# Kernel optimization log

Measured on AMD Instinct MI355X. Metric: run time of the kernel, lower is better.

## Reference

```python
import jax, jax.numpy as jnp
import numpy as np
from jax import lax

B, T, D_IN, H, L, D_OUT = 64, 512, 256, 1024, 3, 128


def setup_inputs() -> dict:
    key = jax.random.key(0)
    ks = jax.random.split(key, 8)
    s_in = 1.0 / np.sqrt(H)  # PyTorch-style uniform-ish scale, keeps ReLU recurrence stable
    return {
        "x": jax.random.normal(ks[0], (B, T, D_IN), jnp.float32),
        "w_ih0": jax.random.normal(ks[1], (H, D_IN), jnp.float32) * s_in,
        "w_ih_rest": jax.random.normal(ks[2], (L - 1, H, H), jnp.float32) * s_in,
        "w_hh": jax.random.normal(ks[3], (L, H, H), jnp.float32) * s_in,
        "b_ih": jax.random.normal(ks[4], (L, H), jnp.float32) * s_in,
        "b_hh": jax.random.normal(ks[5], (L, H), jnp.float32) * s_in,
        "fc_w": jax.random.normal(ks[6], (D_OUT, H), jnp.float32) * s_in,
        "fc_b": jax.random.normal(ks[7], (D_OUT,), jnp.float32) * s_in,
    }


def _rnn_layer(seq, w_ih, w_hh, bi, bh):
    # seq: [B, T, d_in]; precompute input projection as one big GEMM
    pre = jnp.einsum("btd,hd->bth", seq, w_ih) + bi + bh  # [B, T, H]
    h0 = jnp.zeros((seq.shape[0], w_hh.shape[0]), seq.dtype)

    def step(h, p_t):  # h: [B, H], p_t: [B, H]
        h = jax.nn.relu(p_t + h @ w_hh.T)
        return h, h

    _, hs = lax.scan(step, h0, jnp.swapaxes(pre, 0, 1))  # [T, B, H]
    return jnp.swapaxes(hs, 0, 1)  # [B, T, H]


def reference(x, w_ih0, w_ih_rest, w_hh, b_ih, b_hh, fc_w, fc_b):
    seq = _rnn_layer(x, w_ih0, w_hh[0], b_ih[0], b_hh[0])
    for l in range(1, L):
        seq = _rnn_layer(seq, w_ih_rest[l - 1], w_hh[l], b_ih[l], b_hh[l])
    # fc on last timestep: out[:, -1, :] @ fc_w.T + fc_b
    return seq[:, -1, :] @ fc_w.T + fc_b
```

## Files before the change

### kernel.cpp

```cpp
#include <hip/hip_runtime.h>

#define NB   64
#define NT   512
#define DIN  256
#define NH   1024
#define DOUT 128

#define HS2_STR 1156
#define RD_STR  136

typedef float f4 __attribute__((ext_vector_type(4)));
typedef unsigned short bfr;

__device__ __forceinline__ float b2f(bfr u) {
    union { unsigned u; float f; } v; v.u = ((unsigned)u) << 16; return v.f;
}
__device__ __forceinline__ bfr f2b(float f) {
    union { float f; unsigned u; } v; v.f = f;
    unsigned r = v.u + 0x7FFFu + ((v.u >> 16) & 1u);
    return (bfr)(r >> 16);
}

template <typename T> __device__ __forceinline__ f4 load4(const T* p);
template <> __device__ __forceinline__ f4 load4<float>(const float* p) { return *(const f4*)p; }
template <> __device__ __forceinline__ f4 load4<bfr>(const bfr* p) {
    ushort4 u = *(const ushort4*)p;
    f4 r; r[0] = b2f(u.x); r[1] = b2f(u.y); r[2] = b2f(u.z); r[3] = b2f(u.w); return r;
}
template <typename T> __device__ __forceinline__ void store1(T* p, float v);
template <> __device__ __forceinline__ void store1<float>(float* p, float v) { *p = v; }
template <> __device__ __forceinline__ void store1<bfr>(bfr* p, float v) { *p = f2b(v); }
template <typename T> __device__ __forceinline__ float load1(const T* p);
template <> __device__ __forceinline__ float load1<float>(const float* p) { return *p; }
template <> __device__ __forceinline__ float load1<bfr>(const bfr* p) { return b2f(*p); }

template <int K, int LOG2CT, typename TA, typename TO>
__global__ __launch_bounds__(256)
void proj_kernel(const TA* __restrict__ A, const float* __restrict__ W,
                 const float* __restrict__ bih, const float* __restrict__ bhh,
                 TO* __restrict__ out, int tOff)
{
    __shared__ float As[16][68];
    __shared__ float Ws[16][68];
    const int tid = threadIdx.x;
    const int CTM = (1 << LOG2CT) - 1;
    const int m0 = (blockIdx.x >> 4) << 6;
    const int n0 = (blockIdx.x & 15) << 6;
    const int tm = tid & 15, tn = tid >> 4;
    const int lr = tid >> 2, lc = tid & 3;

    const int rA = m0 + lr;
    const long mrowA = (long)(rA >> LOG2CT) * NT + tOff + (rA & CTM);

    float acc[4][4] = {};
    for (int k0 = 0; k0 < K; k0 += 16) {
        f4 av = load4<TA>(&A[mrowA * K + k0 + lc * 4]);
        f4 wv = *(const f4*)&W[(n0 + lr) * K + k0 + lc * 4];
        __syncthreads();
        #pragma unroll
        for (int j = 0; j < 4; ++j) {
            As[lc * 4 + j][lr] = av[j];
            Ws[lc * 4 + j][lr] = wv[j];
        }
        __syncthreads();
        #pragma unroll
        for (int k = 0; k < 16; ++k) {
            f4 a = *(const f4*)&As[k][tm * 4];
            f4 w = *(const f4*)&Ws[k][tn * 4];
            #pragma unroll
            for (int i = 0; i < 4; ++i)
                #pragma unroll
                for (int j = 0; j < 4; ++j)
                    acc[i][j] += a[i] * w[j];
        }
    }
    #pragma unroll
    for (int j = 0; j < 4; ++j) {
        const int n = n0 + tn * 4 + j;
        const float bias = bih[n] + bhh[n];
        #pragma unroll
        for (int i = 0; i < 4; ++i)
            store1<TO>(&out[(long)(m0 + tm * 4 + i) * NH + n], acc[i][j] + bias);
    }
}

template <typename TP, int L2CT>
__global__ __launch_bounds__(256)
void copyback_kernel(const TP* __restrict__ Q, TP* __restrict__ P, int tOff)
{
    const int r = blockIdx.x, tid = threadIdx.x;
    const int b = r >> L2CT, t = r & ((1 << L2CT) - 1);
    const TP* q = Q + (long)r * NH;
    TP* p = P + ((long)b * NT + tOff + t) * NH;
    #pragma unroll
    for (int j = 0; j < 4; ++j) p[tid + j * 256] = q[tid + j * 256];
}

__device__ __forceinline__ void poll64(const unsigned* fl, unsigned tgt, int lane)
{
    const unsigned long long* fp = (const unsigned long long*)fl + lane;
    for (;;) {
        unsigned long long v = __hip_atomic_load(fp, __ATOMIC_RELAXED,
                                                 __HIP_MEMORY_SCOPE_AGENT);
        unsigned lo = (unsigned)v, hi = (unsigned)(v >> 32);
        if (__all((int)(lo >= tgt && hi >= tgt))) break;
        __builtin_amdgcn_s_sleep(1);
    }
}

template <typename TP>
__global__ __launch_bounds__(512)
void recur_kernel(const float* __restrict__ Whh, TP* __restrict__ P,
                  float* __restrict__ Hring, unsigned* __restrict__ sy)
{
    __shared__ float hsA[8 * HS2_STR];
    __shared__ float hsB[8 * HS2_STR];
    __shared__ float red[32 * RD_STR];

    const int tid  = threadIdx.x;
    const int wg   = blockIdx.x;
    const int nBase = (wg & 63) << 4;
    const int set   = wg >> 6;
    const int rank  = wg & 63;
    const int lane  = tid & 63;
    const int tk = tid >> 4, tn = (tid >> 1) & 7, tb = tid & 1;
    const int bl = tid >> 4, nl = tid & 15;
    const int srow = tid >> 6;
    const int sgOff = srow * NH + lane * 4;
    const int slOff = srow * HS2_STR + lane * 4 + ((lane >> 3) << 2);

    unsigned* syA = sy + (set * 2 + 0) * 128;
    unsigned* syB = sy + (set * 2 + 1) * 128;
    float* HrA = Hring + (long)(set * 16) * NH;
    float* HrB = HrA + 8 * NH;

    float w0[32], w1[32];
    {
        const float* p0 = &Whh[(nBase + tn * 2 + 0) * NH + tk * 32];
        const float* p1 = &Whh[(nBase + tn * 2 + 1) * NH + tk * 32];
        #pragma unroll
        for (int i = 0; i < 8; ++i) {
            *(f4*)&w0[i * 4] = *(const f4*)&p0[i * 4];
            *(f4*)&w1[i * 4] = *(const f4*)&p1[i * 4];
        }
    }
    for (int i = tid; i < 8 * HS2_STR; i += 512) { hsA[i] = 0.f; hsB[i] = 0.f; }
    __syncthreads();

    #pragma unroll 1
    for (int ts = 0; ts < NT; ++ts) {
        const int slot = (ts & 1) * (NB * NH);
        const int pslot = ((ts - 1) & 1) * (NB * NH);

        float preA = 0.f, preB = 0.f; TP *ppA = nullptr, *ppB = nullptr;
        if (tid < 128) {
            ppA = &P[((long)(set * 16 + bl) * NT + ts) * NH + nBase + nl];
            ppB = &P[((long)(set * 16 + 8 + bl) * NT + ts) * NH + nBase + nl];
            preA = load1<TP>(ppA);
            preB = load1<TP>(ppB);
        }

        float accA[4][2] = {};
        #pragma unroll
        for (int kk = 0; kk < 8; ++kk) {
            const int kko = tk * 36 + kk * 4;
            f4 hv[4];
            #pragma unroll
            for (int i = 0; i < 4; ++i)
                hv[i] = *(const f4*)&hsA[(tb * 4 + i) * HS2_STR + kko];
            #pragma unroll
            for (int c = 0; c < 4; ++c)
                #pragma unroll
                for (int i = 0; i < 4; ++i) {
                    accA[i][0] += hv[i][c] * w0[kk * 4 + c];
                    accA[i][1] += hv[i][c] * w1[kk * 4 + c];
                }
        }

        f4 sB[4];
        if (ts > 0) {
            poll64(syB, (unsigned)ts, lane);
            const float* src = HrB + pslot + sgOff;
            #pragma unroll
            for (int q = 0; q < 4; ++q)
                asm volatile("global_load_dwordx4 %0, %1, off sc0 sc1"
                             : "=v"(sB[q]) : "v"(src + q * 256) : "memory");
        }

        #pragma unroll
        for (int i = 0; i < 4; ++i) {
            float* rp = &red[tk * RD_STR + (tb * 4 + i) * 16 + tn * 2];
            rp[0] = accA[i][0]; rp[1] = accA[i][1];
        }
        __syncthreads();

        if (tid < 128) {
            float s = 0.f;
            #pragma unroll
            for (int q = 0; q < 32; ++q) s += red[q * RD_STR + tid];
            const float h = fmaxf(s + preA, 0.f);
            store1<TP>(ppA, h);
            __hip_atomic_store(&HrA[slot + bl * NH + nBase + nl], h,
                               __ATOMIC_RELAXED, __HIP_MEMORY_SCOPE_AGENT);
            if (ts < NT - 1) {
                asm volatile("s_waitcnt vmcnt(0)" ::: "memory");
                if (lane == 0)
                    __hip_atomic_store(&syA[rank * 2 + (tid >> 6)], (unsigned)(ts + 1),
                                       __ATOMIC_RELAXED, __HIP_MEMORY_SCOPE_AGENT);
            }
        }

        if (ts > 0) {
            asm volatile("s_waitcnt vmcnt(0)" ::: "memory");
            #pragma unroll
            for (int q = 0; q < 4; ++q)
                *(f4*)&hsB[slOff + q * 288] = sB[q];
        }
        __syncthreads();

        float accB[4][2] = {};
        #pragma unroll
        for (int kk = 0; kk < 8; ++kk) {
            const int kko = tk * 36 + kk * 4;
            f4 hv[4];
            #pragma unroll
            for (int i = 0; i < 4; ++i)
                hv[i] = *(const f4*)&hsB[(tb * 4 + i) * HS2_STR + kko];
            #pragma unroll
            for (int c = 0; c < 4; ++c)
                #pragma unroll
                for (int i = 0; i < 4; ++i) {
                    accB[i][0] += hv[i][c] * w0[kk * 4 + c];
                    accB[i][1] += hv[i][c] * w1[kk * 4 + c];
                }
        }

        f4 sA[4];
        if (ts < NT - 1) {
            poll64(syA, (unsigned)(ts + 1), lane);
            const float* src = HrA + slot + sgOff;
            #pragma unroll
            for (int q = 0; q < 4; ++q)
                asm volatile("global_load_dwordx4 %0, %1, off sc0 sc1"
                             : "=v"(sA[q]) : "v"(src + q * 256) : "memory");
        }

        #pragma unroll
        for (int i = 0; i < 4; ++i) {
            float* rp = &red[tk * RD_STR + (tb * 4 + i) * 16 + tn * 2];
            rp[0] = accB[i][0]; rp[1] = accB[i][1];
        }
        __syncthreads();

        if (tid < 128) {
            float s = 0.f;
            #pragma unroll
            for (int q = 0; q < 32; ++q) s += red[q * RD_STR + tid];
            const float h = fmaxf(s + preB, 0.f);
            store1<TP>(ppB, h);
            __hip_atomic_store(&HrB[slot + bl * NH + nBase + nl], h,
                               __ATOMIC_RELAXED, __HIP_MEMORY_SCOPE_AGENT);
            if (ts < NT - 1) {
                asm volatile("s_waitcnt vmcnt(0)" ::: "memory");
                if (lane == 0)
                    __hip_atomic_store(&syB[rank * 2 + (tid >> 6)], (unsigned)(ts + 1),
                                       __ATOMIC_RELAXED, __HIP_MEMORY_SCOPE_AGENT);
            }
        }
        if (ts == NT - 1) break;

        asm volatile("s_waitcnt vmcnt(0)" ::: "memory");
        #pragma unroll
        for (int q = 0; q < 4; ++q)
            *(f4*)&hsA[slOff + q * 288] = sA[q];
        __syncthreads();
    }
}

template <typename TP>
__global__ __launch_bounds__(128)
void fc_kernel(const TP* __restrict__ seq, const float* __restrict__ fcw,
               const float* __restrict__ fcb, float* __restrict__ out)
{
    __shared__ float hrow[NH];
    const int b = blockIdx.x, tid = threadIdx.x;
    for (int i = tid * 4; i < NH; i += 128 * 4) {
        f4 v = load4<TP>(&seq[((long)b * NT + (NT - 1)) * NH + i]);
        *(f4*)&hrow[i] = v;
    }
    __syncthreads();
    float s = 0.f;
    const float* wr = &fcw[tid * NH];
    for (int k = 0; k < NH; k += 4) {
        f4 w = *(const f4*)&wr[k];
        s += w[0] * hrow[k] + w[1] * hrow[k + 1] + w[2] * hrow[k + 2] + w[3] * hrow[k + 3];
    }
    out[b * DOUT + tid] = s + fcb[tid];
}

template <typename TP>
static void coop_recur(const float* W, TP* P, float* Hring, unsigned* sy,
                       hipStream_t stream)
{
    hipMemsetAsync(sy, 0, 4096, stream);
    const float* Wp = W; TP* Pp = P; float* H = Hring; unsigned* s = sy;
    void* args[4] = { &Wp, &Pp, &H, &s };
    hipLaunchCooperativeKernel((const void*)recur_kernel<TP>, dim3(256), dim3(512),
                               args, 0, stream);
}

static void run_pathA(const float* x, const float* wih0, const float* wihr,
                      const float* whh, const float* bih, const float* bhh,
                      const float* fcw, const float* fcb, float* out,
                      unsigned* sy, float* Hring, float* P0, float* P1,
                      hipStream_t stream)
{
    const dim3 blk(256);
    proj_kernel<DIN, 9, float, float><<<8192, blk, 0, stream>>>(x, wih0, bih, bhh, P0, 0);
    coop_recur<float>(whh, P0, Hring, sy, stream);
    proj_kernel<NH, 9, float, float><<<8192, blk, 0, stream>>>(P0, wihr,
        bih + NH, bhh + NH, P1, 0);
    coop_recur<float>(whh + NH * NH, P1, Hring, sy, stream);
    proj_kernel<NH, 9, float, float><<<8192, blk, 0, stream>>>(P1, wihr + NH * NH,
        bih + 2 * NH, bhh + 2 * NH, P0, 0);
    coop_recur<float>(whh + 2 * (NH * NH), P0, Hring, sy, stream);
    fc_kernel<float><<<dim3(NB), dim3(128), 0, stream>>>(P0, fcw, fcb, out);
}

template <typename TP>
static void run_pathBC(const float* x, const float* wih0, const float* wihr,
                       const float* whh, const float* bih, const float* bhh,
                       const float* fcw, const float* fcb, float* out,
                       unsigned* sy, float* Hring, TP* P, TP* Q, hipStream_t stream)
{
    const dim3 blk(256);
    proj_kernel<DIN, 9, float, TP><<<8192, blk, 0, stream>>>(x, wih0, bih, bhh, P, 0);
    coop_recur<TP>(whh, P, Hring, sy, stream);
    for (int l = 1; l < 3; ++l) {
        const float* wih = wihr + (long)(l - 1) * NH * NH;
        for (int c = 0; c < NT / 32; ++c) {
            proj_kernel<NH, 5, TP, TP><<<512, blk, 0, stream>>>(P, wih, bih + l * NH,
                                                                bhh + l * NH, Q, c * 32);
            copyback_kernel<TP, 5><<<NB * 32, blk, 0, stream>>>(Q, P, c * 32);
        }
        coop_recur<TP>(whh + (long)l * NH * NH, P, Hring, sy, stream);
    }
    fc_kernel<TP><<<dim3(NB), dim3(128), 0, stream>>>(P, fcw, fcb, out);
}

extern "C" void kernel_launch(void* const* d_in, const int* in_sizes, int n_in,
                              void* d_out, int out_size, void* d_ws, size_t ws_size,
                              hipStream_t stream)
{
    (void)in_sizes; (void)n_in; (void)out_size;
    const float* x    = (const float*)d_in[0];
    const float* wih0 = (const float*)d_in[1];
    const float* wihr = (const float*)d_in[2];
    const float* whh  = (const float*)d_in[3];
    const float* bih  = (const float*)d_in[4];
    const float* bhh  = (const float*)d_in[5];
    const float* fcw  = (const float*)d_in[6];
    const float* fcb  = (const float*)d_in[7];
    float* out = (float*)d_out;

    char* ws = (char*)d_ws;
    unsigned* sy = (unsigned*)ws;
    float* Hring = (float*)(ws + 4096);
    char* base = ws + 4096 + 2ull * NB * NH * 4;

    const size_t pF32 = (size_t)NB * NT * NH * 4;
    const size_t qF32 = (size_t)NB * 32 * NH * 4;
    const size_t head = 4096 + 2ull * NB * NH * 4;
    const size_t needA = head + 2 * pF32;
    const size_t needB = head + pF32 + qF32;

    if (ws_size >= needA) {
        float* P0 = (float*)base;
        float* P1 = (float*)(base + pF32);
        run_pathA(x, wih0, wihr, whh, bih, bhh, fcw, fcb, out,
                  sy, Hring, P0, P1, stream);
    } else if (ws_size >= needB) {
        float* P = (float*)base;
        float* Q = (float*)(base + pF32);
        run_pathBC<float>(x, wih0, wihr, whh, bih, bhh, fcw, fcb, out,
                          sy, Hring, P, Q, stream);
    } else {
        bfr* P = (bfr*)base;
        bfr* Q = (bfr*)(base + pF32 / 2);
        run_pathBC<bfr>(x, wih0, wihr, whh, bih, bhh, fcw, fcb, out,
                        sy, Hring, P, Q, stream);
    }
}
```

Baseline: 10.90 ms.

## Fuse all three RNN layers into one wavefront-pipelined cooperative kernel with fp16 state

Replaces the per-layer projection GEMMs and three separate cooperative recurrence launches with one cooperative kernel. It runs the three layers as a diagonal wavefront, with layer l at step g-l, and computes the layer 1 and 2 input projections inline using register-resident W_ih slices. Hidden states are exchanged between workgroups as packed fp16 instead of fp32, which halves the ring traffic and LDS footprint. This removes the large intermediate projection GEMMs, the P buffer round trips and two kernel launches. The cost is three times the per-thread weight registers (160 floats), extra flag polling per step, and reduced precision in the recurrent state.

```diff
diff --git a/kernel.cpp b/kernel.cpp
--- a/kernel.cpp
+++ b/kernel.cpp
@@ -5,9 +5,7 @@
 #define DIN  256
 #define NH   1024
 #define DOUT 128
-
-#define HS2_STR 1156
-#define RD_STR  136
+#define NSTEP (NT + 2)
 
 typedef float f4 __attribute__((ext_vector_type(4)));
 typedef unsigned short bfr;
@@ -19,6 +17,14 @@
     union { float f; unsigned u; } v; v.f = f;
     unsigned r = v.u + 0x7FFFu + ((v.u >> 16) & 1u);
     return (bfr)(r >> 16);
+}
+__device__ __forceinline__ unsigned packh(float a, float b) {
+    union { ushort s; _Float16 f; } x, y;
+    x.f = (_Float16)a; y.f = (_Float16)b;
+    return (unsigned)x.s | ((unsigned)y.s << 16);
+}
+__device__ __forceinline__ float h2f(ushort u) {
+    union { ushort s; _Float16 f; } x; x.s = u; return (float)x.f;
 }
 
 template <typename T> __device__ __forceinline__ f4 load4(const T* p);
@@ -34,27 +40,23 @@
 template <> __device__ __forceinline__ float load1<float>(const float* p) { return *p; }
 template <> __device__ __forceinline__ float load1<bfr>(const bfr* p) { return b2f(*p); }
 
-template <int K, int LOG2CT, typename TA, typename TO>
+template <int K, typename TA, typename TO>
 __global__ __launch_bounds__(256)
 void proj_kernel(const TA* __restrict__ A, const float* __restrict__ W,
                  const float* __restrict__ bih, const float* __restrict__ bhh,
-                 TO* __restrict__ out, int tOff)
+                 TO* __restrict__ out)
 {
     __shared__ float As[16][68];
     __shared__ float Ws[16][68];
     const int tid = threadIdx.x;
-    const int CTM = (1 << LOG2CT) - 1;
     const int m0 = (blockIdx.x >> 4) << 6;
     const int n0 = (blockIdx.x & 15) << 6;
     const int tm = tid & 15, tn = tid >> 4;
     const int lr = tid >> 2, lc = tid & 3;
 
-    const int rA = m0 + lr;
-    const long mrowA = (long)(rA >> LOG2CT) * NT + tOff + (rA & CTM);
-
     float acc[4][4] = {};
     for (int k0 = 0; k0 < K; k0 += 16) {
-        f4 av = load4<TA>(&A[mrowA * K + k0 + lc * 4]);
+        f4 av = load4<TA>(&A[(long)(m0 + lr) * K + k0 + lc * 4]);
         f4 wv = *(const f4*)&W[(n0 + lr) * K + k0 + lc * 4];
         __syncthreads();
         #pragma unroll
@@ -84,18 +86,6 @@
     }
 }
 
-template <typename TP, int L2CT>
-__global__ __launch_bounds__(256)
-void copyback_kernel(const TP* __restrict__ Q, TP* __restrict__ P, int tOff)
-{
-    const int r = blockIdx.x, tid = threadIdx.x;
-    const int b = r >> L2CT, t = r & ((1 << L2CT) - 1);
-    const TP* q = Q + (long)r * NH;
-    TP* p = P + ((long)b * NT + tOff + t) * NH;
-    #pragma unroll
-    for (int j = 0; j < 4; ++j) p[tid + j * 256] = q[tid + j * 256];
-}
-
 __device__ __forceinline__ void poll64(const unsigned* fl, unsigned tgt, int lane)
 {
     const unsigned long long* fp = (const unsigned long long*)fl + lane;
@@ -108,185 +98,227 @@
     }
 }
 
-template <typename TP>
+__device__ __forceinline__ float mixrow(const ushort* hbase, const float* w, float acc)
+{
+    const uint4* hp = (const uint4*)hbase;
+    uint4 c0 = hp[0], c1 = hp[1], c2 = hp[2], c3 = hp[3];
+    unsigned uu[16] = { c0.x, c0.y, c0.z, c0.w, c1.x, c1.y, c1.z, c1.w,
+                        c2.x, c2.y, c2.z, c2.w, c3.x, c3.y, c3.z, c3.w };
+    #pragma unroll
+    for (int j = 0; j < 16; ++j) {
+        union { unsigned u; _Float16 h[2]; } t; t.u = uu[j];
+        acc = fmaf((float)t.h[0], w[2 * j + 0], acc);
+        acc = fmaf((float)t.h[1], w[2 * j + 1], acc);
+    }
+    return acc;
+}
+
+template <typename TP0>
 __global__ __launch_bounds__(512)
-void recur_kernel(const float* __restrict__ Whh, TP* __restrict__ P,
-                  float* __restrict__ Hring, unsigned* __restrict__ sy)
-{
-    __shared__ float hsA[8 * HS2_STR];
-    __shared__ float hsB[8 * HS2_STR];
-    __shared__ float red[32 * RD_STR];
+void fused_kernel(const float* __restrict__ whh, const float* __restrict__ wih1,
+                  const float* __restrict__ wih2, const float* __restrict__ bih,
+                  const float* __restrict__ bhh, const TP0* __restrict__ P0,
+                  ushort* __restrict__ Hr, unsigned* __restrict__ sy)
+{
+    __shared__ ushort hs0[16 * NH];
+    __shared__ ushort hs1[16 * NH];
+    __shared__ ushort hs2[16 * NH];
+    __shared__ float red[32][260];
 
     const int tid  = threadIdx.x;
     const int wg   = blockIdx.x;
-    const int nBase = (wg & 63) << 4;
-    const int set   = wg >> 6;
-    const int rank  = wg & 63;
-    const int lane  = tid & 63;
-    const int tk = tid >> 4, tn = (tid >> 1) & 7, tb = tid & 1;
-    const int bl = tid >> 4, nl = tid & 15;
-    const int srow = tid >> 6;
-    const int sgOff = srow * NH + lane * 4;
-    const int slOff = srow * HS2_STR + lane * 4 + ((lane >> 3) << 2);
-
-    unsigned* syA = sy + (set * 2 + 0) * 128;
-    unsigned* syB = sy + (set * 2 + 1) * 128;
-    float* HrA = Hring + (long)(set * 16) * NH;
-    float* HrB = HrA + 8 * NH;
-
-    float w0[32], w1[32];
+    const int rank = wg & 63, set = wg >> 6, lane = tid & 63;
+    const int nBase = rank << 4;
+    const int tk = tid >> 4, tn = tid & 15;
+    const int ko = tk << 5;
+
+    float w0[32], wA[32], w1[32], wB[32], w2[32];
     {
-        const float* p0 = &Whh[(nBase + tn * 2 + 0) * NH + tk * 32];
-        const float* p1 = &Whh[(nBase + tn * 2 + 1) * NH + tk * 32];
+        const long ro = (long)(nBase + tn) * NH + ko;
         #pragma unroll
-        for (int i = 0; i < 8; ++i) {
-            *(f4*)&w0[i * 4] = *(const f4*)&p0[i * 4];
-            *(f4*)&w1[i * 4] = *(const f4*)&p1[i * 4];
-        }
-    }
-    for (int i = tid; i < 8 * HS2_STR; i += 512) { hsA[i] = 0.f; hsB[i] = 0.f; }
+        for (int j = 0; j < 8; ++j) {
+            *(f4*)&w0[j * 4] = *(const f4*)&whh[ro + j * 4];
+            *(f4*)&w1[j * 4] = *(const f4*)&whh[(long)NH * NH + ro + j * 4];
+            *(f4*)&w2[j * 4] = *(const f4*)&whh[2L * NH * NH + ro + j * 4];
+            *(f4*)&wA[j * 4] = *(const f4*)&wih1[ro + j * 4];
+            *(f4*)&wB[j * 4] = *(const f4*)&wih2[ro + j * 4];
+        }
+    }
+    const int rb = tid >> 3, rp = tid & 7;
+    const int n2 = nBase + rp * 2;
+    float bs10 = 0, bs11 = 0, bs20 = 0, bs21 = 0;
+    if (tid < 128) {
+        bs10 = bih[NH + n2] + bhh[NH + n2];
+        bs11 = bih[NH + n2 + 1] + bhh[NH + n2 + 1];
+        bs20 = bih[2 * NH + n2] + bhh[2 * NH + n2];
+        bs21 = bih[2 * NH + n2 + 1] + bhh[2 * NH + n2 + 1];
+    }
+    for (int i = tid; i < 16 * NH / 2; i += 512) {
+        ((unsigned*)hs0)[i] = 0; ((unsigned*)hs1)[i] = 0; ((unsigned*)hs2)[i] = 0;
+    }
     __syncthreads();
 
+    unsigned* fl0 = sy + (set * 3 + 0) * 128;
+    unsigned* fl1 = sy + (set * 3 + 1) * 128;
+    unsigned* fl2 = sy + (set * 3 + 2) * 128;
+    ushort* H0 = Hr;
+    ushort* H1 = Hr + 2 * 65536;
+    ushort* H2 = Hr + 4 * 65536;
+    const int sOff = set * 16384 + tid * 32;
+    const long pBase = ((long)set * 16 + rb) * NT;
+    const int oIdx = rb * 16 + rp * 2;
+
     #pragma unroll 1
-    for (int ts = 0; ts < NT; ++ts) {
-        const int slot = (ts & 1) * (NB * NH);
-        const int pslot = ((ts - 1) & 1) * (NB * NH);
-
-        float preA = 0.f, preB = 0.f; TP *ppA = nullptr, *ppB = nullptr;
-        if (tid < 128) {
-            ppA = &P[((long)(set * 16 + bl) * NT + ts) * NH + nBase + nl];
-            ppB = &P[((long)(set * 16 + 8 + bl) * NT + ts) * NH + nBase + nl];
-            preA = load1<TP>(ppA);
-            preB = load1<TP>(ppB);
-        }
-
-        float accA[4][2] = {};
-        #pragma unroll
-        for (int kk = 0; kk < 8; ++kk) {
-            const int kko = tk * 36 + kk * 4;
-            f4 hv[4];
-            #pragma unroll
-            for (int i = 0; i < 4; ++i)
-                hv[i] = *(const f4*)&hsA[(tb * 4 + i) * HS2_STR + kko];
-            #pragma unroll
-            for (int c = 0; c < 4; ++c)
-                #pragma unroll
-                for (int i = 0; i < 4; ++i) {
-                    accA[i][0] += hv[i][c] * w0[kk * 4 + c];
-                    accA[i][1] += hv[i][c] * w1[kk * 4 + c];
-                }
-        }
-
-        f4 sB[4];
-        if (ts > 0) {
-            poll64(syB, (unsigned)ts, lane);
-            const float* src = HrB + pslot + sgOff;
+    for (int g = 0; g < NSTEP; ++g) {
+        const int slot = g & 1, oslot = slot ^ 1;
+        const bool a0 = (g <= NT - 1);
+        const bool a1 = (g >= 1) && (g <= NT);
+        const bool a2 = (g >= 2) && (g <= NT + 1);
+        const bool sg1 = (g >= 2) && (g <= NT + 1);
+        const bool sg2 = (g >= 3) && (g <= NT + 1);
+        const bool sg0 = (g <= NT - 1);
+        float acc[16];
+        f4 st[4];
+
+        float p00 = 0.f, p01 = 0.f;
+        if (a0 && tid < 128) {
+            const long pa = (pBase + g) * NH + n2;
+            p00 = load1<TP0>(&P0[pa]); p01 = load1<TP0>(&P0[pa + 1]);
+        }
+        if (a0) {
+            #pragma unroll
+            for (int b = 0; b < 16; ++b)
+                acc[b] = mixrow(&hs0[b * NH + ko], w0, 0.f);
+        }
+        if (sg1) {
+            poll64(fl1, (unsigned)g, lane);
+            const char* sp = (const char*)(H1 + oslot * 65536 + sOff);
             #pragma unroll
             for (int q = 0; q < 4; ++q)
                 asm volatile("global_load_dwordx4 %0, %1, off sc0 sc1"
-                             : "=v"(sB[q]) : "v"(src + q * 256) : "memory");
-        }
-
-        #pragma unroll
-        for (int i = 0; i < 4; ++i) {
-            float* rp = &red[tk * RD_STR + (tb * 4 + i) * 16 + tn * 2];
-            rp[0] = accA[i][0]; rp[1] = accA[i][1];
-        }
-        __syncthreads();
-
-        if (tid < 128) {
-            float s = 0.f;
-            #pragma unroll
-            for (int q = 0; q < 32; ++q) s += red[q * RD_STR + tid];
-            const float h = fmaxf(s + preA, 0.f);
-            store1<TP>(ppA, h);
-            __hip_atomic_store(&HrA[slot + bl * NH + nBase + nl], h,
-                               __ATOMIC_RELAXED, __HIP_MEMORY_SCOPE_AGENT);
-            if (ts < NT - 1) {
-                asm volatile("s_waitcnt vmcnt(0)" ::: "memory");
-                if (lane == 0)
-                    __hip_atomic_store(&syA[rank * 2 + (tid >> 6)], (unsigned)(ts + 1),
-                                       __ATOMIC_RELAXED, __HIP_MEMORY_SCOPE_AGENT);
+                             : "=v"(st[q]) : "v"(sp + q * 16) : "memory");
+        }
+        if (a0) {
+            #pragma unroll
+            for (int b = 0; b < 16; ++b) red[tk][b * 16 + tn] = acc[b];
+        }
+        __syncthreads();
+        if (a0 && tid < 128) {
+            float s0 = 0.f, s1 = 0.f;
+            #pragma unroll
+            for (int q = 0; q < 32; ++q) { s0 += red[q][oIdx]; s1 += red[q][oIdx + 1]; }
+            const float v0 = fmaxf(s0 + p00, 0.f), v1 = fmaxf(s1 + p01, 0.f);
+            __hip_atomic_store((unsigned*)(H0 + slot * 65536 + ((set * 16 + rb) << 10) + n2),
+                               packh(v0, v1), __ATOMIC_RELAXED, __HIP_MEMORY_SCOPE_AGENT);
+            asm volatile("s_waitcnt vmcnt(0)" ::: "memory");
+            if (lane == 0)
+                __hip_atomic_store(&fl0[rank * 2 + (tid >> 6)], (unsigned)(g + 1),
+                                   __ATOMIC_RELAXED, __HIP_MEMORY_SCOPE_AGENT);
+        }
+        if (sg1) {
+            asm volatile("s_waitcnt vmcnt(0)" ::: "memory");
+            char* dp = (char*)hs1 + tid * 64;
+            #pragma unroll
+            for (int q = 0; q < 4; ++q) *(f4*)(dp + q * 16) = st[q];
+        }
+        __syncthreads();
+
+        if (a1) {
+            #pragma unroll
+            for (int b = 0; b < 16; ++b) {
+                float a = mixrow(&hs0[b * NH + ko], wA, 0.f);
+                acc[b] = mixrow(&hs1[b * NH + ko], w1, a);
             }
         }
-
-        if (ts > 0) {
-            asm volatile("s_waitcnt vmcnt(0)" ::: "memory");
-            #pragma unroll
-            for (int q = 0; q < 4; ++q)
-                *(f4*)&hsB[slOff + q * 288] = sB[q];
-        }
-        __syncthreads();
-
-        float accB[4][2] = {};
-        #pragma unroll
-        for (int kk = 0; kk < 8; ++kk) {
-            const int kko = tk * 36 + kk * 4;
-            f4 hv[4];
-            #pragma unroll
-            for (int i = 0; i < 4; ++i)
-                hv[i] = *(const f4*)&hsB[(tb * 4 + i) * HS2_STR + kko];
-            #pragma unroll
-            for (int c = 0; c < 4; ++c)
-                #pragma unroll
-                for (int i = 0; i < 4; ++i) {
-                    accB[i][0] += hv[i][c] * w0[kk * 4 + c];
-                    accB[i][1] += hv[i][c] * w1[kk * 4 + c];
-                }
-        }
-
-        f4 sA[4];
-        if (ts < NT - 1) {
-            poll64(syA, (unsigned)(ts + 1), lane);
-            const float* src = HrA + slot + sgOff;
+        if (sg2) {
+            poll64(fl2, (unsigned)g, lane);
+            const char* sp = (const char*)(H2 + oslot * 65536 + sOff);
             #pragma unroll
             for (int q = 0; q < 4; ++q)
                 asm volatile("global_load_dwordx4 %0, %1, off sc0 sc1"
-                             : "=v"(sA[q]) : "v"(src + q * 256) : "memory");
-        }
-
-        #pragma unroll
-        for (int i = 0; i < 4; ++i) {
-            float* rp = &red[tk * RD_STR + (tb * 4 + i) * 16 + tn * 2];
-            rp[0] = accB[i][0]; rp[1] = accB[i][1];
-        }
-        __syncthreads();
-
-        if (tid < 128) {
-            float s = 0.f;
-            #pragma unroll
-            for (int q = 0; q < 32; ++q) s += red[q * RD_STR + tid];
-            const float h = fmaxf(s + preB, 0.f);
-            store1<TP>(ppB, h);
-            __hip_atomic_store(&HrB[slot + bl * NH + nBase + nl], h,
-                               __ATOMIC_RELAXED, __HIP_MEMORY_SCOPE_AGENT);
-            if (ts < NT - 1) {
-                asm volatile("s_waitcnt vmcnt(0)" ::: "memory");
-                if (lane == 0)
-                    __hip_atomic_store(&syB[rank * 2 + (tid >> 6)], (unsigned)(ts + 1),
-                                       __ATOMIC_RELAXED, __HIP_MEMORY_SCOPE_AGENT);
+                             : "=v"(st[q]) : "v"(sp + q * 16) : "memory");
+        }
+        if (a1) {
+            #pragma unroll
+            for (int b = 0; b < 16; ++b) red[tk][b * 16 + tn] = acc[b];
+        }
+        __syncthreads();
+        if (a1 && tid < 128) {
+            float s0 = 0.f, s1 = 0.f;
+            #pragma unroll
+            for (int q = 0; q < 32; ++q) { s0 += red[q][oIdx]; s1 += red[q][oIdx + 1]; }
+            const float v0 = fmaxf(s0 + bs10, 0.f), v1 = fmaxf(s1 + bs11, 0.f);
+            __hip_atomic_store((unsigned*)(H1 + slot * 65536 + ((set * 16 + rb) << 10) + n2),
+                               packh(v0, v1), __ATOMIC_RELAXED, __HIP_MEMORY_SCOPE_AGENT);
+            asm volatile("s_waitcnt vmcnt(0)" ::: "memory");
+            if (lane == 0)
+                __hip_atomic_store(&fl1[rank * 2 + (tid >> 6)], (unsigned)(g + 1),
+                                   __ATOMIC_RELAXED, __HIP_MEMORY_SCOPE_AGENT);
+        }
+        if (sg2) {
+            asm volatile("s_waitcnt vmcnt(0)" ::: "memory");
+            char* dp = (char*)hs2 + tid * 64;
+            #pragma unroll
+            for (int q = 0; q < 4; ++q) *(f4*)(dp + q * 16) = st[q];
+        }
+        __syncthreads();
+
+        if (a2) {
+            #pragma unroll
+            for (int b = 0; b < 16; ++b) {
+                float a = mixrow(&hs1[b * NH + ko], wB, 0.f);
+                acc[b] = mixrow(&hs2[b * NH + ko], w2, a);
             }
         }
-        if (ts == NT - 1) break;
-
-        asm volatile("s_waitcnt vmcnt(0)" ::: "memory");
-        #pragma unroll
-        for (int q = 0; q < 4; ++q)
-            *(f4*)&hsA[slOff + q * 288] = sA[q];
-        __syncthreads();
-    }
-}
-
-template <typename TP>
+        if (sg0) {
+            poll64(fl0, (unsigned)(g + 1), lane);
+            const char* sp = (const char*)(H0 + slot * 65536 + sOff);
+            #pragma unroll
+            for (int q = 0; q < 4; ++q)
+                asm volatile("global_load_dwordx4 %0, %1, off sc0 sc1"
+                             : "=v"(st[q]) : "v"(sp + q * 16) : "memory");
+        }
+        if (a2) {
+            #pragma unroll
+            for (int b = 0; b < 16; ++b) red[tk][b * 16 + tn] = acc[b];
+        }
+        __syncthreads();
+        if (a2 && tid < 128) {
+            float s0 = 0.f, s1 = 0.f;
+            #pragma unroll
+            for (int q = 0; q < 32; ++q) { s0 += red[q][oIdx]; s1 += red[q][oIdx + 1]; }
+            const float v0 = fmaxf(s0 + bs20, 0.f), v1 = fmaxf(s1 + bs21, 0.f);
+            __hip_atomic_store((unsigned*)(H2 + slot * 65536 + ((set * 16 + rb) << 10) + n2),
+                               packh(v0, v1), __ATOMIC_RELAXED, __HIP_MEMORY_SCOPE_AGENT);
+            asm volatile("s_waitcnt vmcnt(0)" ::: "memory");
+            if (lane == 0)
+                __hip_atomic_store(&fl2[rank * 2 + (tid >> 6)], (unsigned)(g + 1),
+                                   __ATOMIC_RELAXED, __HIP_MEMORY_SCOPE_AGENT);
+        }
+        if (sg0) {
+            asm volatile("s_waitcnt vmcnt(0)" ::: "memory");
+            char* dp = (char*)hs0 + tid * 64;
+            #pragma unroll
+            for (int q = 0; q < 4; ++q) *(f4*)(dp + q * 16) = st[q];
+        }
+        __syncthreads();
+    }
+}
+
 __global__ __launch_bounds__(128)
-void fc_kernel(const TP* __restrict__ seq, const float* __restrict__ fcw,
-               const float* __restrict__ fcb, float* __restrict__ out)
+void fc16_kernel(const ushort* __restrict__ h2, const float* __restrict__ fcw,
+                 const float* __restrict__ fcb, float* __restrict__ out)
 {
     __shared__ float hrow[NH];
     const int b = blockIdx.x, tid = threadIdx.x;
-    for (int i = tid * 4; i < NH; i += 128 * 4) {
-        f4 v = load4<TP>(&seq[((long)b * NT + (NT - 1)) * NH + i]);
-        *(f4*)&hrow[i] = v;
+    const ushort* src = h2 + (b << 10);
+    #pragma unroll
+    for (int j = 0; j < 2; ++j) {
+        ushort4 u = *(const ushort4*)&src[tid * 8 + j * 4];
+        hrow[tid * 8 + j * 4 + 0] = h2f(u.x);
+        hrow[tid * 8 + j * 4 + 1] = h2f(u.y);
+        hrow[tid * 8 + j * 4 + 2] = h2f(u.z);
+        hrow[tid * 8 + j * 4 + 3] = h2f(u.w);
     }
     __syncthreads();
     float s = 0.f;
@@ -298,54 +330,18 @@
     out[b * DOUT + tid] = s + fcb[tid];
 }
 
-template <typename TP>
-static void coop_recur(const float* W, TP* P, float* Hring, unsigned* sy,
-                       hipStream_t stream)
-{
-    hipMemsetAsync(sy, 0, 4096, stream);
-    const float* Wp = W; TP* Pp = P; float* H = Hring; unsigned* s = sy;
-    void* args[4] = { &Wp, &Pp, &H, &s };
-    hipLaunchCooperativeKernel((const void*)recur_kernel<TP>, dim3(256), dim3(512),
+template <typename TP0>
+static void run_fused(const float* x, const float* wih0, const float* wihr,
+                      const float* whh, const float* bih, const float* bhh,
+                      unsigned* sy, ushort* Hr, TP0* P0, hipStream_t stream)
+{
+    proj_kernel<DIN, float, TP0><<<8192, 256, 0, stream>>>(x, wih0, bih, bhh, P0);
+    const float* wp = whh; const float* wi1 = wihr; const float* wi2 = wihr + NH * NH;
+    const float* bi = bih; const float* bh = bhh;
+    const TP0* Pp = P0; ushort* H = Hr; unsigned* s = sy;
+    void* args[8] = { &wp, &wi1, &wi2, &bi, &bh, &Pp, &H, &s };
+    hipLaunchCooperativeKernel((const void*)fused_kernel<TP0>, dim3(256), dim3(512),
                                args, 0, stream);
-}
-
-static void run_pathA(const float* x, const float* wih0, const float* wihr,
-                      const float* whh, const float* bih, const float* bhh,
-                      const float* fcw, const float* fcb, float* out,
-                      unsigned* sy, float* Hring, float* P0, float* P1,
-                      hipStream_t stream)
-{
-    const dim3 blk(256);
-    proj_kernel<DIN, 9, float, float><<<8192, blk, 0, stream>>>(x, wih0, bih, bhh, P0, 0);
-    coop_recur<float>(whh, P0, Hring, sy, stream);
-    proj_kernel<NH, 9, float, float><<<8192, blk, 0, stream>>>(P0, wihr,
-        bih + NH, bhh + NH, P1, 0);
-    coop_recur<float>(whh + NH * NH, P1, Hring, sy, stream);
-    proj_kernel<NH, 9, float, float><<<8192, blk, 0, stream>>>(P1, wihr + NH * NH,
-        bih + 2 * NH, bhh + 2 * NH, P0, 0);
-    coop_recur<float>(whh + 2 * (NH * NH), P0, Hring, sy, stream);
-    fc_kernel<float><<<dim3(NB), dim3(128), 0, stream>>>(P0, fcw, fcb, out);
-}
-
-template <typename TP>
-static void run_pathBC(const float* x, const float* wih0, const float* wihr,
-                       const float* whh, const float* bih, const float* bhh,
-                       const float* fcw, const float* fcb, float* out,
-                       unsigned* sy, float* Hring, TP* P, TP* Q, hipStream_t stream)
-{
-    const dim3 blk(256);
-    proj_kernel<DIN, 9, float, TP><<<8192, blk, 0, stream>>>(x, wih0, bih, bhh, P, 0);
-    coop_recur<TP>(whh, P, Hring, sy, stream);
-    for (int l = 1; l < 3; ++l) {
-        const float* wih = wihr + (long)(l - 1) * NH * NH;
-        for (int c = 0; c < NT / 32; ++c) {
-            proj_kernel<NH, 5, TP, TP><<<512, blk, 0, stream>>>(P, wih, bih + l * NH,
-                                                                bhh + l * NH, Q, c * 32);
-            copyback_kernel<TP, 5><<<NB * 32, blk, 0, stream>>>(Q, P, c * 32);
-        }
-        coop_recur<TP>(whh + (long)l * NH * NH, P, Hring, sy, stream);
-    }
-    fc_kernel<TP><<<dim3(NB), dim3(128), 0, stream>>>(P, fcw, fcb, out);
 }
 
 extern "C" void kernel_launch(void* const* d_in, const int* in_sizes, int n_in,
@@ -365,29 +361,15 @@
 
     char* ws = (char*)d_ws;
     unsigned* sy = (unsigned*)ws;
-    float* Hring = (float*)(ws + 4096);
-    char* base = ws + 4096 + 2ull * NB * NH * 4;
+    ushort* Hr = (ushort*)(ws + 8192);
+    char* base = ws + (1 << 20);
 
     const size_t pF32 = (size_t)NB * NT * NH * 4;
-    const size_t qF32 = (size_t)NB * 32 * NH * 4;
-    const size_t head = 4096 + 2ull * NB * NH * 4;
-    const size_t needA = head + 2 * pF32;
-    const size_t needB = head + pF32 + qF32;
-
-    if (ws_size >= needA) {
-        float* P0 = (float*)base;
-        float* P1 = (float*)(base + pF32);
-        run_pathA(x, wih0, wihr, whh, bih, bhh, fcw, fcb, out,
-                  sy, Hring, P0, P1, stream);
-    } else if (ws_size >= needB) {
-        float* P = (float*)base;
-        float* Q = (float*)(base + pF32);
-        run_pathBC<float>(x, wih0, wihr, whh, bih, bhh, fcw, fcb, out,
-                          sy, Hring, P, Q, stream);
+    hipMemsetAsync(sy, 0, 8192, stream);
+    if (ws_size >= (size_t)(1 << 20) + pF32) {
+        run_fused<float>(x, wih0, wihr, whh, bih, bhh, sy, Hr, (float*)base, stream);
     } else {
-        bfr* P = (bfr*)base;
-        bfr* Q = (bfr*)(base + pF32 / 2);
-        run_pathBC<bfr>(x, wih0, wihr, whh, bih, bhh, fcw, fcb, out,
-                        sy, Hring, P, Q, stream);
-    }
-}
+        run_fused<bfr>(x, wih0, wihr, whh, bih, bhh, sy, Hr, (bfr*)base, stream);
+    }
+    fc16_kernel<<<dim3(NB), dim3(128), 0, stream>>>(Hr + 5 * 65536, fcw, fcb, out);
+}
```

After: 33.01 ms. +202.9%, slower.
